# Kernel tuning notes

Measured on AMD Instinct MI355X. Metric: run time of the kernel, lower is better.

## Reference

```python
import jax, jax.numpy as jnp
import numpy as np

B, S, T, D = 32, 128, 65536, 768
VOCAB, N_SEC, N_TEMP, N_NEG, MAX_SENT, N_TS = 30522, 6, 3, 2, 128, 512
LN_EPS = 1e-5


def setup_inputs() -> dict:
    key = jax.random.key(0)
    ks = jax.random.split(key, 16)
    return {
        "token_ids": jax.random.randint(ks[0], (T,), 0, VOCAB),
        "segment_ids": jnp.sort(jax.random.randint(ks[1], (T,), 0, B * S)),
        "section_ids": jax.random.randint(ks[2], (B, S), 0, N_SEC),
        "temporality_ids": jax.random.randint(ks[3], (B, S), 0, N_TEMP),
        "negation_ids": jax.random.randint(ks[4], (B, S), 0, N_NEG),
        "position_ids": jax.random.randint(ks[5], (B, S), 0, MAX_SENT),
        "timestamp_ids": jax.random.randint(ks[6], (B, S), 0, N_TS),
        "token_table": jax.random.normal(ks[7], (VOCAB, D), jnp.float32),
        "section_table": jax.random.normal(ks[8], (N_SEC, D), jnp.float32),
        "temporality_table": jax.random.normal(ks[9], (N_TEMP, D), jnp.float32),
        "negation_table": jax.random.normal(ks[10], (N_NEG, D), jnp.float32),
        "position_table": jax.random.normal(ks[11], (MAX_SENT, D), jnp.float32),
        "timestamp_table": jax.random.normal(ks[12], (N_TS, D), jnp.float32),
        "ln_gamma": jnp.ones((D,), jnp.float32),
        "ln_beta": jnp.zeros((D,), jnp.float32),
        "proj_w": jax.random.normal(ks[13], (D, D), jnp.float32) * (1.0 / np.sqrt(D)),
        "proj_b": jnp.zeros((D,), jnp.float32),
    }


def reference(token_ids, segment_ids, section_ids, temporality_ids, negation_ids,
              position_ids, timestamp_ids, token_table, section_table,
              temporality_table, negation_table, position_table, timestamp_table,
              ln_gamma, ln_beta, proj_w, proj_b):
    # ragged per-sentence token-embedding mean pool (segment mean over B*S slots)
    tok = token_table[token_ids]                                  # [T, D]
    sums = jax.ops.segment_sum(tok, segment_ids, num_segments=B * S)
    cnt = jax.ops.segment_sum(jnp.ones((T,), tok.dtype), segment_ids,
                              num_segments=B * S)
    base = (sums / jnp.maximum(cnt, 1.0)[:, None]).reshape(B, S, D)
    # multi-embedding sum
    enriched = (base
                + section_table[section_ids]
                + temporality_table[temporality_ids]
                + negation_table[negation_ids]
                + position_table[position_ids]
                + timestamp_table[timestamp_ids])                 # [B, S, D]
    # LayerNorm + Linear
    mu = enriched.mean(-1, keepdims=True)
    var = jnp.mean(jnp.square(enriched - mu), axis=-1, keepdims=True)
    normed = (enriched - mu) * jax.lax.rsqrt(var + LN_EPS) * ln_gamma + ln_beta
    tokens = jnp.einsum('bsd,ed->bse', normed, proj_w) + proj_b   # [B, S, D]
    padding_mask = jnp.zeros((B, S), dtype=bool)                  # all sentences valid
    return tokens, padding_mask
```

## Files before the change

### kernel.cpp

```cpp
#include <hip/hip_runtime.h>
#include <stdint.h>

#define Tn 65536
#define Dn 768
#define NSEG 4096

typedef __bf16 bf16;
typedef __bf16 bf16x8 __attribute__((ext_vector_type(8)));
typedef float f32x4 __attribute__((ext_vector_type(4)));

__device__ inline float block_sum192(float v, float* sm) {
  #pragma unroll
  for (int o = 32; o > 0; o >>= 1) v += __shfl_down(v, o, 64);
  const int lane = threadIdx.x & 63, w = threadIdx.x >> 6;
  __syncthreads();
  if (lane == 0) sm[w] = v;
  __syncthreads();
  return sm[0] + sm[1] + sm[2];
}

__global__ __launch_bounds__(192) void k_pool_ln(
    const int* __restrict__ token_ids, const int* __restrict__ segment_ids,
    const int* __restrict__ section_ids, const int* __restrict__ temporality_ids,
    const int* __restrict__ negation_ids, const int* __restrict__ position_ids,
    const int* __restrict__ timestamp_ids,
    const float* __restrict__ token_table, const float* __restrict__ section_table,
    const float* __restrict__ temporality_table, const float* __restrict__ negation_table,
    const float* __restrict__ position_table, const float* __restrict__ timestamp_table,
    const float* __restrict__ gamma, const float* __restrict__ beta,
    bf16* __restrict__ out_normed)
{
  const int n = blockIdx.x;
  const int tid = threadIdx.x;
  __shared__ float red[3];

  int lo = 0, hi = Tn;
  while (lo < hi) { int mid = (lo + hi) >> 1; if (segment_ids[mid] < n) lo = mid + 1; else hi = mid; }
  const int start = lo;
  hi = Tn;
  while (lo < hi) { int mid = (lo + hi) >> 1; if (segment_ids[mid] < n + 1) lo = mid + 1; else hi = mid; }
  const int end = lo;
  const float scale = 1.0f / fmaxf((float)(end - start), 1.0f);

  float4 acc = make_float4(0.f, 0.f, 0.f, 0.f);
  for (int t = start; t < end; ++t) {
    const int tok = token_ids[t];
    const float4 v = *(const float4*)(token_table + (size_t)tok * Dn + 4 * tid);
    acc.x += v.x; acc.y += v.y; acc.z += v.z; acc.w += v.w;
  }

  const int sec = section_ids[n];
  const int tmp = temporality_ids[n];
  const int neg = negation_ids[n];
  const int pos = position_ids[n];
  const int ts  = timestamp_ids[n];
  const float4 v1 = *(const float4*)(section_table     + (size_t)sec * Dn + 4 * tid);
  const float4 v2 = *(const float4*)(temporality_table + (size_t)tmp * Dn + 4 * tid);
  const float4 v3 = *(const float4*)(negation_table    + (size_t)neg * Dn + 4 * tid);
  const float4 v4 = *(const float4*)(position_table    + (size_t)pos * Dn + 4 * tid);
  const float4 v5 = *(const float4*)(timestamp_table   + (size_t)ts  * Dn + 4 * tid);

  float4 e;
  e.x = acc.x * scale + v1.x + v2.x + v3.x + v4.x + v5.x;
  e.y = acc.y * scale + v1.y + v2.y + v3.y + v4.y + v5.y;
  e.z = acc.z * scale + v1.z + v2.z + v3.z + v4.z + v5.z;
  e.w = acc.w * scale + v1.w + v2.w + v3.w + v4.w + v5.w;

  const float mu = block_sum192(e.x + e.y + e.z + e.w, red) * (1.0f / 768.0f);
  const float dx = e.x - mu, dy = e.y - mu, dz = e.z - mu, dw = e.w - mu;
  const float var = block_sum192(dx*dx + dy*dy + dz*dz + dw*dw, red) * (1.0f / 768.0f);
  const float inv = rsqrtf(var + 1e-5f);

  const float4 g = *(const float4*)(gamma + 4 * tid);
  const float4 b = *(const float4*)(beta  + 4 * tid);
  alignas(8) bf16 o[4];
  o[0] = (bf16)(dx * inv * g.x + b.x);
  o[1] = (bf16)(dy * inv * g.y + b.y);
  o[2] = (bf16)(dz * inv * g.z + b.z);
  o[3] = (bf16)(dw * inv * g.w + b.w);
  *(ushort4*)(out_normed + (size_t)n * Dn + 4 * tid) = *(ushort4*)o;
}

__global__ __launch_bounds__(256) void k_cvt_w(const float* __restrict__ w,
                                               bf16* __restrict__ wb) {
  const int i = blockIdx.x * 256 + threadIdx.x;
  const float4 v = ((const float4*)w)[i];
  alignas(8) bf16 o[4] = {(bf16)v.x, (bf16)v.y, (bf16)v.z, (bf16)v.w};
  ((ushort4*)wb)[i] = *(ushort4*)o;
}

__global__ __launch_bounds__(256) void k_mask(float* __restrict__ out) {
  out[blockIdx.x * 256 + threadIdx.x] = 0.0f;
}

__global__ __launch_bounds__(256) void k_gemm(
    const bf16* __restrict__ A, const bf16* __restrict__ W,
    const float* __restrict__ bias, float* __restrict__ out)
{
  __shared__ bf16 As[128 * 32];
  __shared__ bf16 Bs[128 * 32];
  const int tid  = threadIdx.x;
  const int lane = tid & 63;
  const int w    = tid >> 6;
  const int m0 = blockIdx.y * 128;
  const int n0 = blockIdx.x * 128;
  const int wm = (w >> 1) * 64;
  const int wn = (w & 1) * 64;

  f32x4 acc[4][4];
  #pragma unroll
  for (int i = 0; i < 4; ++i)
    #pragma unroll
    for (int j = 0; j < 4; ++j) acc[i][j] = (f32x4){0.f, 0.f, 0.f, 0.f};

  const int fr = tid >> 2;
  const int fc = (tid & 3) * 8;
  const bf16* agp = A + (size_t)(m0 + fr) * 768 + fc;
  const bf16* bgp = W + (size_t)(n0 + fr) * 768 + fc;

  for (int kt = 0; kt < 24; ++kt) {
    __syncthreads();
    #pragma unroll
    for (int it = 0; it < 2; ++it) {
      const int f = it * 256 + tid;
      __builtin_amdgcn_global_load_lds(
          (const __attribute__((address_space(1))) void*)(agp + (size_t)it * 64 * 768 + kt * 32),
          (__attribute__((address_space(3))) void*)(As + f * 8), 16, 0, 0);
      __builtin_amdgcn_global_load_lds(
          (const __attribute__((address_space(1))) void*)(bgp + (size_t)it * 64 * 768 + kt * 32),
          (__attribute__((address_space(3))) void*)(Bs + f * 8), 16, 0, 0);
    }
    __syncthreads();

    bf16x8 af[4], bfr[4];
    #pragma unroll
    for (int i = 0; i < 4; ++i)
      af[i] = *(const bf16x8*)(As + (wm + i * 16 + (lane & 15)) * 32 + (lane >> 4) * 8);
    #pragma unroll
    for (int j = 0; j < 4; ++j)
      bfr[j] = *(const bf16x8*)(Bs + (wn + j * 16 + (lane & 15)) * 32 + (lane >> 4) * 8);

    #pragma unroll
    for (int i = 0; i < 4; ++i)
      #pragma unroll
      for (int j = 0; j < 4; ++j)
        acc[i][j] = __builtin_amdgcn_mfma_f32_16x16x32_bf16(af[i], bfr[j], acc[i][j], 0, 0, 0);
  }

  float bvals[4];
  #pragma unroll
  for (int j = 0; j < 4; ++j) bvals[j] = bias[n0 + wn + j * 16 + (lane & 15)];
  const int r0 = (lane >> 4) * 4;
  #pragma unroll
  for (int i = 0; i < 4; ++i) {
    #pragma unroll
    for (int r = 0; r < 4; ++r) {
      const int gm = m0 + wm + i * 16 + r0 + r;
      float* orow = out + (size_t)gm * 768 + n0 + wn;
      #pragma unroll
      for (int j = 0; j < 4; ++j)
        orow[j * 16 + (lane & 15)] = acc[i][j][r] + bvals[j];
    }
  }
}

extern "C" void kernel_launch(void* const* d_in, const int* in_sizes, int n_in,
                              void* d_out, int out_size, void* d_ws, size_t ws_size,
                              hipStream_t stream) {
  const int* token_ids       = (const int*)d_in[0];
  const int* segment_ids     = (const int*)d_in[1];
  const int* section_ids     = (const int*)d_in[2];
  const int* temporality_ids = (const int*)d_in[3];
  const int* negation_ids    = (const int*)d_in[4];
  const int* position_ids    = (const int*)d_in[5];
  const int* timestamp_ids   = (const int*)d_in[6];
  const float* token_table       = (const float*)d_in[7];
  const float* section_table     = (const float*)d_in[8];
  const float* temporality_table = (const float*)d_in[9];
  const float* negation_table    = (const float*)d_in[10];
  const float* position_table    = (const float*)d_in[11];
  const float* timestamp_table   = (const float*)d_in[12];
  const float* ln_gamma = (const float*)d_in[13];
  const float* ln_beta  = (const float*)d_in[14];
  const float* proj_w   = (const float*)d_in[15];
  const float* proj_b   = (const float*)d_in[16];

  float* out = (float*)d_out;
  bf16* wsW = (bf16*)d_ws;
  bf16* wsN = (bf16*)d_ws + (size_t)Dn * Dn;

  k_cvt_w<<<576, 256, 0, stream>>>(proj_w, wsW);
  k_pool_ln<<<NSEG, 192, 0, stream>>>(token_ids, segment_ids, section_ids,
      temporality_ids, negation_ids, position_ids, timestamp_ids,
      token_table, section_table, temporality_table, negation_table,
      position_table, timestamp_table, ln_gamma, ln_beta, wsN);
  k_mask<<<16, 256, 0, stream>>>(out + (size_t)NSEG * Dn);
  k_gemm<<<dim3(6, 32), 256, 0, stream>>>(wsN, wsW, proj_b, out);
}
```

Baseline: 219.1 us.

## Unroll token gather, fuse mask into weight convert, halve GEMM M-tile

```diff
diff --git a/kernel.cpp b/kernel.cpp
--- a/kernel.cpp
+++ b/kernel.cpp
@@ -8,6 +8,10 @@
 typedef __bf16 bf16;
 typedef __bf16 bf16x8 __attribute__((ext_vector_type(8)));
 typedef float f32x4 __attribute__((ext_vector_type(4)));
+
+__device__ inline void f4add(float4& a, const float4& v) {
+  a.x += v.x; a.y += v.y; a.z += v.z; a.w += v.w;
+}
 
 __device__ inline float block_sum192(float v, float* sm) {
   #pragma unroll
@@ -42,13 +46,6 @@
   const int end = lo;
   const float scale = 1.0f / fmaxf((float)(end - start), 1.0f);
 
-  float4 acc = make_float4(0.f, 0.f, 0.f, 0.f);
-  for (int t = start; t < end; ++t) {
-    const int tok = token_ids[t];
-    const float4 v = *(const float4*)(token_table + (size_t)tok * Dn + 4 * tid);
-    acc.x += v.x; acc.y += v.y; acc.z += v.z; acc.w += v.w;
-  }
-
   const int sec = section_ids[n];
   const int tmp = temporality_ids[n];
   const int neg = negation_ids[n];
@@ -60,11 +57,31 @@
   const float4 v4 = *(const float4*)(position_table    + (size_t)pos * Dn + 4 * tid);
   const float4 v5 = *(const float4*)(timestamp_table   + (size_t)ts  * Dn + 4 * tid);
 
+  const float4* tt = (const float4*)token_table;
+  float4 a0 = make_float4(0.f,0.f,0.f,0.f), a1 = a0, a2 = a0, a3 = a0;
+  int t = start;
+  for (; t + 4 <= end; t += 4) {
+    const int i0 = token_ids[t + 0];
+    const int i1 = token_ids[t + 1];
+    const int i2 = token_ids[t + 2];
+    const int i3 = token_ids[t + 3];
+    const float4 w0 = tt[(size_t)i0 * 192 + tid];
+    const float4 w1 = tt[(size_t)i1 * 192 + tid];
+    const float4 w2 = tt[(size_t)i2 * 192 + tid];
+    const float4 w3 = tt[(size_t)i3 * 192 + tid];
+    f4add(a0, w0); f4add(a1, w1); f4add(a2, w2); f4add(a3, w3);
+  }
+  for (; t < end; ++t) {
+    const float4 w0 = tt[(size_t)token_ids[t] * 192 + tid];
+    f4add(a0, w0);
+  }
+  f4add(a0, a1); f4add(a2, a3); f4add(a0, a2);
+
   float4 e;
-  e.x = acc.x * scale + v1.x + v2.x + v3.x + v4.x + v5.x;
-  e.y = acc.y * scale + v1.y + v2.y + v3.y + v4.y + v5.y;
-  e.z = acc.z * scale + v1.z + v2.z + v3.z + v4.z + v5.z;
-  e.w = acc.w * scale + v1.w + v2.w + v3.w + v4.w + v5.w;
+  e.x = a0.x * scale + v1.x + v2.x + v3.x + v4.x + v5.x;
+  e.y = a0.y * scale + v1.y + v2.y + v3.y + v4.y + v5.y;
+  e.z = a0.z * scale + v1.z + v2.z + v3.z + v4.z + v5.z;
+  e.w = a0.w * scale + v1.w + v2.w + v3.w + v4.w + v5.w;
 
   const float mu = block_sum192(e.x + e.y + e.z + e.w, red) * (1.0f / 768.0f);
   const float dx = e.x - mu, dy = e.y - mu, dz = e.z - mu, dw = e.w - mu;
@@ -81,35 +98,37 @@
   *(ushort4*)(out_normed + (size_t)n * Dn + 4 * tid) = *(ushort4*)o;
 }
 
-__global__ __launch_bounds__(256) void k_cvt_w(const float* __restrict__ w,
-                                               bf16* __restrict__ wb) {
-  const int i = blockIdx.x * 256 + threadIdx.x;
-  const float4 v = ((const float4*)w)[i];
-  alignas(8) bf16 o[4] = {(bf16)v.x, (bf16)v.y, (bf16)v.z, (bf16)v.w};
-  ((ushort4*)wb)[i] = *(ushort4*)o;
-}
-
-__global__ __launch_bounds__(256) void k_mask(float* __restrict__ out) {
-  out[blockIdx.x * 256 + threadIdx.x] = 0.0f;
+__global__ __launch_bounds__(256) void k_cvt_mask(const float* __restrict__ w,
+                                                  bf16* __restrict__ wb,
+                                                  float* __restrict__ mask_out) {
+  const int b = blockIdx.x;
+  if (b < 576) {
+    const int i = b * 256 + threadIdx.x;
+    const float4 v = ((const float4*)w)[i];
+    alignas(8) bf16 o[4] = {(bf16)v.x, (bf16)v.y, (bf16)v.z, (bf16)v.w};
+    ((ushort4*)wb)[i] = *(ushort4*)o;
+  } else {
+    mask_out[(b - 576) * 256 + threadIdx.x] = 0.0f;
+  }
 }
 
 __global__ __launch_bounds__(256) void k_gemm(
     const bf16* __restrict__ A, const bf16* __restrict__ W,
     const float* __restrict__ bias, float* __restrict__ out)
 {
-  __shared__ bf16 As[128 * 32];
+  __shared__ bf16 As[64 * 32];
   __shared__ bf16 Bs[128 * 32];
   const int tid  = threadIdx.x;
   const int lane = tid & 63;
   const int w    = tid >> 6;
-  const int m0 = blockIdx.y * 128;
+  const int m0 = blockIdx.y * 64;
   const int n0 = blockIdx.x * 128;
-  const int wm = (w >> 1) * 64;
+  const int wm = (w >> 1) * 32;
   const int wn = (w & 1) * 64;
 
-  f32x4 acc[4][4];
-  #pragma unroll
-  for (int i = 0; i < 4; ++i)
+  f32x4 acc[2][4];
+  #pragma unroll
+  for (int i = 0; i < 2; ++i)
     #pragma unroll
     for (int j = 0; j < 4; ++j) acc[i][j] = (f32x4){0.f, 0.f, 0.f, 0.f};
 
@@ -120,28 +139,28 @@
 
   for (int kt = 0; kt < 24; ++kt) {
     __syncthreads();
+    __builtin_amdgcn_global_load_lds(
+        (const __attribute__((address_space(1))) void*)(agp + kt * 32),
+        (__attribute__((address_space(3))) void*)(As + tid * 8), 16, 0, 0);
     #pragma unroll
     for (int it = 0; it < 2; ++it) {
       const int f = it * 256 + tid;
-      __builtin_amdgcn_global_load_lds(
-          (const __attribute__((address_space(1))) void*)(agp + (size_t)it * 64 * 768 + kt * 32),
-          (__attribute__((address_space(3))) void*)(As + f * 8), 16, 0, 0);
       __builtin_amdgcn_global_load_lds(
           (const __attribute__((address_space(1))) void*)(bgp + (size_t)it * 64 * 768 + kt * 32),
           (__attribute__((address_space(3))) void*)(Bs + f * 8), 16, 0, 0);
     }
     __syncthreads();
 
-    bf16x8 af[4], bfr[4];
-    #pragma unroll
-    for (int i = 0; i < 4; ++i)
+    bf16x8 af[2], bfr[4];
+    #pragma unroll
+    for (int i = 0; i < 2; ++i)
       af[i] = *(const bf16x8*)(As + (wm + i * 16 + (lane & 15)) * 32 + (lane >> 4) * 8);
     #pragma unroll
     for (int j = 0; j < 4; ++j)
       bfr[j] = *(const bf16x8*)(Bs + (wn + j * 16 + (lane & 15)) * 32 + (lane >> 4) * 8);
 
     #pragma unroll
-    for (int i = 0; i < 4; ++i)
+    for (int i = 0; i < 2; ++i)
       #pragma unroll
       for (int j = 0; j < 4; ++j)
         acc[i][j] = __builtin_amdgcn_mfma_f32_16x16x32_bf16(af[i], bfr[j], acc[i][j], 0, 0, 0);
@@ -152,7 +171,7 @@
   for (int j = 0; j < 4; ++j) bvals[j] = bias[n0 + wn + j * 16 + (lane & 15)];
   const int r0 = (lane >> 4) * 4;
   #pragma unroll
-  for (int i = 0; i < 4; ++i) {
+  for (int i = 0; i < 2; ++i) {
     #pragma unroll
     for (int r = 0; r < 4; ++r) {
       const int gm = m0 + wm + i * 16 + r0 + r;
@@ -189,11 +208,10 @@
   bf16* wsW = (bf16*)d_ws;
   bf16* wsN = (bf16*)d_ws + (size_t)Dn * Dn;
 
-  k_cvt_w<<<576, 256, 0, stream>>>(proj_w, wsW);
+  k_cvt_mask<<<592, 256, 0, stream>>>(proj_w, wsW, out + (size_t)NSEG * Dn);
   k_pool_ln<<<NSEG, 192, 0, stream>>>(token_ids, segment_ids, section_ids,
       temporality_ids, negation_ids, position_ids, timestamp_ids,
       token_table, section_table, temporality_table, negation_table,
       position_table, timestamp_table, ln_gamma, ln_beta, wsN);
-  k_mask<<<16, 256, 0, stream>>>(out + (size_t)NSEG * Dn);
-  k_gemm<<<dim3(6, 32), 256, 0, stream>>>(wsN, wsW, proj_b, out);
-}
+  k_gemm<<<dim3(6, 64), 256, 0, stream>>>(wsN, wsW, proj_b, out);
+}
```

Result: faster. 209.3 us (-4.4%).
